# Optimization experiments

Measured on AMD Instinct MI355X. Metric: run time of the kernel, lower is better.

## Reference

```python
import jax, jax.numpy as jnp
import numpy as np

C = 768
HEADS = 12

def setup_inputs() -> dict:
    key = jax.random.key(0)
    k1, k2, k3 = jax.random.split(key, 3)
    x = jax.random.normal(k1, (8, C, 32, 32), dtype=jnp.float32)
    # 1x1 convs are channel-wise linear maps; store as [out_c, in_c]
    w_qkv = jax.random.normal(k2, (3 * C, C), dtype=jnp.float32) * (C ** -0.5)
    w_proj = jax.random.normal(k3, (C, C), dtype=jnp.float32) * (C ** -0.5)
    return {"x": x, "w_qkv": w_qkv, "w_proj": w_proj}

def reference(x, w_qkv, w_proj):
    b, c, h, w = x.shape
    heads = HEADS
    dh = c // heads
    n = h * w
    scale = dh ** -0.5
    # 1x1 conv QKV: [b, 3c, h, w] -> [b, 3, heads, dh, n]
    qkv = jnp.einsum('oc,bchw->bohw', w_qkv, x).reshape(b, 3, heads, dh, n)
    q, k, v = qkv[:, 0], qkv[:, 1], qkv[:, 2]  # each [b, heads, dh, n]
    attn = jnp.einsum('bhdn,bhdm->bhnm', q, k) * scale  # [b, heads, n, n]
    attn = jax.nn.softmax(attn, axis=-1)
    out = jnp.einsum('bhnm,bhdm->bhdn', attn, v)  # [b, heads, dh, n]
    out = out.reshape(b, c, h, w)
    return jnp.einsum('oc,bchw->bohw', w_proj, out)
```

## Files before the change

### kernel.cpp

```cpp
#include <hip/hip_runtime.h>

typedef unsigned short u16;
typedef unsigned int u32;
typedef float v4f __attribute__((ext_vector_type(4)));
typedef __bf16 bf16x8 __attribute__((ext_vector_type(8)));

#define BATCH 8
#define CDIM 768
#define NHEAD 12
#define DH 64
#define NSEQ 1024
#define SCL 0.18033688011112042f

__device__ __forceinline__ u16 f2bf(float f) {
  u32 u = __builtin_bit_cast(u32, f);
  u += 0x7fffu + ((u >> 16) & 1u);
  return (u16)(u >> 16);
}

__device__ __forceinline__ u16 b16(float f) {
  return (u16)((__builtin_bit_cast(u32, f) + 0x8000u) >> 16);
}
__device__ __forceinline__ u32 pkbf(float hi, float lo) {
  u32 a = __builtin_bit_cast(u32, hi) + 0x8000u;
  u32 b = __builtin_bit_cast(u32, lo) + 0x8000u;
  return __builtin_amdgcn_perm(a, b, 0x07060302u);
}

__device__ __forceinline__ v4f mfma16(bf16x8 a, bf16x8 b, v4f c) {
  return __builtin_amdgcn_mfma_f32_16x16x32_bf16(a, b, c, 0, 0, 0);
}

__device__ __forceinline__ void gload16(const u16* g, u16* l) {
  __builtin_amdgcn_global_load_lds(
      (const __attribute__((address_space(1))) void*)g,
      (__attribute__((address_space(3))) void*)l, 16, 0, 0);
}

__global__ __launch_bounds__(256) void k_prep(const float* __restrict__ x,
                                              const float* __restrict__ wq,
                                              const float* __restrict__ wp,
                                              u16* __restrict__ xT,
                                              u16* __restrict__ wqb,
                                              u16* __restrict__ wpb) {
  __shared__ u16 Ts[64][72];
  int bid = blockIdx.x;
  int t = threadIdx.x;
  if (bid < 2304) {
    bool isQ = bid < 1728;
    const float* s = isQ ? wq : wp;
    u16* d = isQ ? wqb : wpb;
    int i = (isQ ? bid : bid - 1728) * 256 + t;
    float4 v = ((const float4*)s)[i];
    u32 lo = (u32)f2bf(v.x) | ((u32)f2bf(v.y) << 16);
    u32 hi = (u32)f2bf(v.z) | ((u32)f2bf(v.w) << 16);
    ((uint2*)d)[i] = uint2{lo, hi};
    return;
  }
  int id = bid - 2304;
  int p0 = (id & 15) * 64; id >>= 4;
  int c0 = (id % 12) * 64; int b = id / 12;
  int cr = t >> 4;
  int p4 = (t & 15) * 4;
  const float* src = x + ((size_t)b * CDIM + c0) * NSEQ + p0;
#pragma unroll
  for (int i = 0; i < 4; ++i) {
    int c = cr + i * 16;
    float4 v = *(const float4*)&src[(size_t)c * NSEQ + p4];
    Ts[p4 + 0][c] = f2bf(v.x);
    Ts[p4 + 1][c] = f2bf(v.y);
    Ts[p4 + 2][c] = f2bf(v.z);
    Ts[p4 + 3][c] = f2bf(v.w);
  }
  __syncthreads();
  int p = t >> 2;
  int cq = t & 3;
  u16* dst = xT + ((size_t)b * NSEQ + p0 + p) * CDIM + c0;
#pragma unroll
  for (int j = 0; j < 2; ++j) {
    int ch = cq + j * 4;
    *(int4*)&dst[ch * 8] = *(const int4*)&Ts[p][ch * 8];
  }
}

__global__ __launch_bounds__(256) void k_gemm_qkv(const u16* __restrict__ Wb,
                                                  const u16* __restrict__ xT,
                                                  u16* __restrict__ qkT,
                                                  u16* __restrict__ vbuf) {
  int oT = blockIdx.x * 128, pT = blockIdx.y * 128, b = blockIdx.z;
  __shared__ u16 As[2][128 * 32];
  __shared__ u16 Bs[2][128 * 32];
  int t = threadIdx.x, lane = t & 63, wid = t >> 6;
  int ln = lane & 15, quad = lane >> 4;
  int wr = wid >> 1, wc = wid & 1;
  v4f acc[4][4] = {};

  int lr = lane >> 2, lc = (lane & 3) * 8;
  const u16* Ag = Wb + (size_t)(oT + wid * 16 + lr) * CDIM + lc;
  const u16* Bg = xT + ((size_t)b * NSEQ + pT + wid * 16 + lr) * CDIM + lc;
  int s0 = (wid * 16) * 32, s1 = (wid * 16 + 64) * 32;

  for (int kk = 0; kk < CDIM; kk += 64) {
    __syncthreads();
    gload16(Ag + kk, &As[0][s0]);
    gload16(Ag + (size_t)64 * CDIM + kk, &As[0][s1]);
    gload16(Ag + kk + 32, &As[1][s0]);
    gload16(Ag + (size_t)64 * CDIM + kk + 32, &As[1][s1]);
    gload16(Bg + kk, &Bs[0][s0]);
    gload16(Bg + (size_t)64 * CDIM + kk, &Bs[0][s1]);
    gload16(Bg + kk + 32, &Bs[1][s0]);
    gload16(Bg + (size_t)64 * CDIM + kk + 32, &Bs[1][s1]);
    __syncthreads();

    bf16x8 af0[4], af1[4], bf0[4], bf1[4];
#pragma unroll
    for (int mt = 0; mt < 4; ++mt) {
      af0[mt] = *(const bf16x8*)&As[0][(wr * 64 + mt * 16 + ln) * 32 + quad * 8];
      af1[mt] = *(const bf16x8*)&As[1][(wr * 64 + mt * 16 + ln) * 32 + quad * 8];
    }
#pragma unroll
    for (int nt = 0; nt < 4; ++nt) {
      bf0[nt] = *(const bf16x8*)&Bs[0][(wc * 64 + nt * 16 + ln) * 32 + quad * 8];
      bf1[nt] = *(const bf16x8*)&Bs[1][(wc * 64 + nt * 16 + ln) * 32 + quad * 8];
    }
#pragma unroll
    for (int mt = 0; mt < 4; ++mt)
#pragma unroll
      for (int nt = 0; nt < 4; ++nt) {
        acc[mt][nt] = mfma16(af0[mt], bf0[nt], acc[mt][nt]);
        acc[mt][nt] = mfma16(af1[mt], bf1[nt], acc[mt][nt]);
      }
  }

  bool isV = (oT >= 2 * CDIM);
#pragma unroll
  for (int mt = 0; mt < 4; ++mt) {
#pragma unroll
    for (int nt = 0; nt < 4; ++nt) {
      int ro = oT + wr * 64 + mt * 16 + quad * 4;
      int cp = pT + wc * 64 + nt * 16 + ln;
      if (!isV) {
        u32 lo = (u32)f2bf(acc[mt][nt][0]) | ((u32)f2bf(acc[mt][nt][1]) << 16);
        u32 hi = (u32)f2bf(acc[mt][nt][2]) | ((u32)f2bf(acc[mt][nt][3]) << 16);
        *(uint2*)&qkT[((size_t)b * NSEQ + cp) * 1536 + ro] = uint2{lo, hi};
      } else {
#pragma unroll
        for (int r = 0; r < 4; ++r)
          vbuf[((size_t)b * CDIM + (ro - 2 * CDIM + r)) * NSEQ + cp] =
              f2bf(acc[mt][nt][r]);
      }
    }
  }
}

__global__ __launch_bounds__(256) void k_attn(const u16* __restrict__ qkT,
                                              const u16* __restrict__ vbuf,
                                              u16* __restrict__ attnT) {
  int id = blockIdx.x;
  int b = id & 7;
  int j = id >> 3;
  int h = j % 12;
  int nt0 = (j / 12) * 128;

  int t = threadIdx.x, lane = t & 63, wid = t >> 6;
  int ln = lane & 15, quad = lane >> 4;
  int nbase = nt0 + wid * 32;

  __shared__ u16 Ks[2][2][64 * 32];
  __shared__ u16 Vs[2][2][64 * 32];
  __shared__ u16 Pa[4][32 * 72];
  u16* myP = Pa[wid];

  const u16* qbase = qkT + ((size_t)b * NSEQ + nbase) * 1536 + h * DH;
  bf16x8 aq[2][2];
#pragma unroll
  for (int mt = 0; mt < 2; ++mt)
#pragma unroll
    for (int ks = 0; ks < 2; ++ks)
      aq[mt][ks] = *(const bf16x8*)&qbase[(size_t)(mt * 16 + ln) * 1536 + ks * 32 + quad * 8];

  bf16x8 ones;
#pragma unroll
  for (int i = 0; i < 8; ++i) ones[i] = __builtin_bit_cast(__bf16, (u16)0x3F80);

  v4f oacc[2][4] = {};
  v4f lacc[2] = {};

  int lr = lane >> 2, lc = (lane & 3) * 8;
  const u16* kgw = qkT + (size_t)b * NSEQ * 1536 + CDIM + h * DH +
                   (size_t)(wid * 16 + lr) * 1536 + lc;
  const u16* vgw = vbuf + ((size_t)b * CDIM + h * DH + wid * 16 + lr) * NSEQ + lc;
  int sb = (wid * 16) * 32;

  gload16(kgw, &Ks[0][0][sb]);
  gload16(kgw + 32, &Ks[0][1][sb]);
  gload16(vgw, &Vs[0][0][sb]);
  gload16(vgw + 32, &Vs[0][1][sb]);
  __syncthreads();

  for (int s = 0; s < 16; ++s) {
    int cur = s & 1, nxt = cur ^ 1;
    if (s < 15) {
      size_t ko = (size_t)(s + 1) * 64 * 1536;
      int vo = (s + 1) * 64;
      gload16(kgw + ko, &Ks[nxt][0][sb]);
      gload16(kgw + ko + 32, &Ks[nxt][1][sb]);
      gload16(vgw + vo, &Vs[nxt][0][sb]);
      gload16(vgw + vo + 32, &Vs[nxt][1][sb]);
    }

#pragma unroll
    for (int ct = 0; ct < 4; ++ct) {
      bf16x8 kf0 = *(const bf16x8*)&Ks[cur][0][(ct * 16 + ln) * 32 + quad * 8];
      bf16x8 kf1 = *(const bf16x8*)&Ks[cur][1][(ct * 16 + ln) * 32 + quad * 8];
#pragma unroll
      for (int mt = 0; mt < 2; ++mt) {
        v4f sc = {};
        sc = mfma16(kf0, aq[mt][0], sc);
        sc = mfma16(kf1, aq[mt][1], sc);
        float p0 = __builtin_amdgcn_exp2f(sc[0] * SCL);
        float p1 = __builtin_amdgcn_exp2f(sc[1] * SCL);
        float p2 = __builtin_amdgcn_exp2f(sc[2] * SCL);
        float p3 = __builtin_amdgcn_exp2f(sc[3] * SCL);
        *(uint2*)&myP[(mt * 16 + ln) * 72 + ct * 16 + quad * 4] =
            uint2{pkbf(p1, p0), pkbf(p3, p2)};
      }
    }

    bf16x8 ap[2][2];
#pragma unroll
    for (int mt = 0; mt < 2; ++mt)
#pragma unroll
      for (int ks = 0; ks < 2; ++ks)
        ap[mt][ks] = *(const bf16x8*)&myP[(mt * 16 + ln) * 72 + ks * 32 + quad * 8];
#pragma unroll
    for (int mt = 0; mt < 2; ++mt) {
      lacc[mt] = mfma16(ap[mt][0], ones, lacc[mt]);
      lacc[mt] = mfma16(ap[mt][1], ones, lacc[mt]);
    }
#pragma unroll
    for (int nt = 0; nt < 4; ++nt) {
      bf16x8 vf0 = *(const bf16x8*)&Vs[cur][0][(nt * 16 + ln) * 32 + quad * 8];
      bf16x8 vf1 = *(const bf16x8*)&Vs[cur][1][(nt * 16 + ln) * 32 + quad * 8];
#pragma unroll
      for (int mt = 0; mt < 2; ++mt) {
        oacc[mt][nt] = mfma16(ap[mt][0], vf0, oacc[mt][nt]);
        oacc[mt][nt] = mfma16(ap[mt][1], vf1, oacc[mt][nt]);
      }
    }
    __syncthreads();
  }

#pragma unroll
  for (int mt = 0; mt < 2; ++mt) {
#pragma unroll
    for (int r = 0; r < 4; ++r) {
      float inv = 1.0f / lacc[mt][r];
      int n = nbase + mt * 16 + quad * 4 + r;
      u16* dst = attnT + ((size_t)b * NSEQ + n) * CDIM + h * DH;
#pragma unroll
      for (int nt = 0; nt < 4; ++nt)
        dst[nt * 16 + ln] = b16(oacc[mt][nt][r] * inv);
    }
  }
}

__global__ __launch_bounds__(256) void k_gemm_proj(const u16* __restrict__ Wb,
                                                   const u16* __restrict__ aT,
                                                   float* __restrict__ out) {
  int b = blockIdx.x, oT = blockIdx.y * 128, pT = blockIdx.z * 128;
  __shared__ u16 As[2][128 * 32];
  __shared__ u16 Bs[2][128 * 32];
  int t = threadIdx.x, lane = t & 63, wid = t >> 6;
  int ln = lane & 15, quad = lane >> 4;
  int wr = wid >> 1, wc = wid & 1;
  v4f acc[4][4] = {};

  int lr = lane >> 2, lc = (lane & 3) * 8;
  const u16* Ag = Wb + (size_t)(oT + wid * 16 + lr) * CDIM + lc;
  const u16* Bg = aT + ((size_t)b * NSEQ + pT + wid * 16 + lr) * CDIM + lc;
  int s0 = (wid * 16) * 32, s1 = (wid * 16 + 64) * 32;

  for (int kk = 0; kk < CDIM; kk += 64) {
    __syncthreads();
    gload16(Ag + kk, &As[0][s0]);
    gload16(Ag + (size_t)64 * CDIM + kk, &As[0][s1]);
    gload16(Ag + kk + 32, &As[1][s0]);
    gload16(Ag + (size_t)64 * CDIM + kk + 32, &As[1][s1]);
    gload16(Bg + kk, &Bs[0][s0]);
    gload16(Bg + (size_t)64 * CDIM + kk, &Bs[0][s1]);
    gload16(Bg + kk + 32, &Bs[1][s0]);
    gload16(Bg + (size_t)64 * CDIM + kk + 32, &Bs[1][s1]);
    __syncthreads();

    bf16x8 af0[4], af1[4], bf0[4], bf1[4];
#pragma unroll
    for (int mt = 0; mt < 4; ++mt) {
      af0[mt] = *(const bf16x8*)&As[0][(wr * 64 + mt * 16 + ln) * 32 + quad * 8];
      af1[mt] = *(const bf16x8*)&As[1][(wr * 64 + mt * 16 + ln) * 32 + quad * 8];
    }
#pragma unroll
    for (int nt = 0; nt < 4; ++nt) {
      bf0[nt] = *(const bf16x8*)&Bs[0][(wc * 64 + nt * 16 + ln) * 32 + quad * 8];
      bf1[nt] = *(const bf16x8*)&Bs[1][(wc * 64 + nt * 16 + ln) * 32 + quad * 8];
    }
#pragma unroll
    for (int mt = 0; mt < 4; ++mt)
#pragma unroll
      for (int nt = 0; nt < 4; ++nt) {
        acc[mt][nt] = mfma16(af0[mt], bf0[nt], acc[mt][nt]);
        acc[mt][nt] = mfma16(af1[mt], bf1[nt], acc[mt][nt]);
      }
  }

#pragma unroll
  for (int mt = 0; mt < 4; ++mt) {
#pragma unroll
    for (int nt = 0; nt < 4; ++nt) {
      int ro = oT + wr * 64 + mt * 16 + quad * 4;
      int cp = pT + wc * 64 + nt * 16 + ln;
#pragma unroll
      for (int r = 0; r < 4; ++r)
        out[((size_t)b * CDIM + ro + r) * NSEQ + cp] = acc[mt][nt][r];
    }
  }
}

extern "C" void kernel_launch(void* const* d_in, const int* in_sizes, int n_in,
                              void* d_out, int out_size, void* d_ws, size_t ws_size,
                              hipStream_t stream) {
  const float* x = (const float*)d_in[0];
  const float* w_qkv = (const float*)d_in[1];
  const float* w_proj = (const float*)d_in[2];
  float* out = (float*)d_out;

  char* ws = (char*)d_ws;
  u16* wqkv_bf = (u16*)(ws);
  u16* wproj_bf = (u16*)(ws + 3538944);
  u16* xT = (u16*)(ws + 4718592);
  u16* vbuf = (u16*)(ws + 17301504);
  u16* qkT = (u16*)d_out;
  u16* attnT = xT;

  k_prep<<<dim3(3840), dim3(256), 0, stream>>>(x, w_qkv, w_proj, xT, wqkv_bf, wproj_bf);
  k_gemm_qkv<<<dim3(18, 8, 8), dim3(256), 0, stream>>>(wqkv_bf, xT, qkT, vbuf);
  k_attn<<<dim3(768), dim3(256), 0, stream>>>(qkT, vbuf, attnT);
  k_gemm_proj<<<dim3(8, 6, 8), dim3(256), 0, stream>>>(wproj_bf, attnT, out);
}
```

Baseline: 193.0 us.

## Rewrite QKV and projection GEMMs with triple-buffered pipelined shared-memory core

Both 1x1-conv GEMMs now share one core: 512-thread blocks computing 128x256 tiles, a three-stage LDS ring filled by direct global-to-LDS loads, XOR-swizzled LDS layout against bank conflicts, split MFMA phases with raised wave priority, and explicit waitcnt/barrier scheduling. The grid is flattened with a block-index swizzle for L2 locality, and tiles may span batch boundaries. The aim is to hide global load latency behind MFMA work and raise per-block reuse. In exchange it uses about 144KB of LDS per block and relies on hand-placed waitcnt counts being correct.

Result: no change. 190.8 us (-1.2%).

```diff
diff --git a/kernel.cpp b/kernel.cpp
--- a/kernel.cpp
+++ b/kernel.cpp
@@ -21,6 +21,7 @@
 __device__ __forceinline__ u16 b16(float f) {
   return (u16)((__builtin_bit_cast(u32, f) + 0x8000u) >> 16);
 }
+
 __device__ __forceinline__ u32 pkbf(float hi, float lo) {
   u32 a = __builtin_bit_cast(u32, hi) + 0x8000u;
   u32 b = __builtin_bit_cast(u32, lo) + 0x8000u;
@@ -83,71 +84,151 @@
   }
 }
 
-__global__ __launch_bounds__(256) void k_gemm_qkv(const u16* __restrict__ Wb,
-                                                  const u16* __restrict__ xT,
-                                                  u16* __restrict__ qkT,
-                                                  u16* __restrict__ vbuf) {
-  int oT = blockIdx.x * 128, pT = blockIdx.y * 128, b = blockIdx.z;
-  __shared__ u16 As[2][128 * 32];
-  __shared__ u16 Bs[2][128 * 32];
+#define NKT 12
+
+__device__ __forceinline__ void gemm_core(const u16* __restrict__ Ag,
+                                          const u16* __restrict__ Bg,
+                                          u16* sm, v4f (&acc)[4][4]) {
   int t = threadIdx.x, lane = t & 63, wid = t >> 6;
   int ln = lane & 15, quad = lane >> 4;
-  int wr = wid >> 1, wc = wid & 1;
+  int wm = wid >> 2, wn = wid & 3;
+
+  int sr = t >> 3;
+  int sc = ((t & 7) ^ (sr & 7)) * 8;
+  const u16* As0 = Ag + (size_t)sr * CDIM + sc;
+  const u16* Bs0 = Bg + (size_t)sr * CDIM + sc;
+  int ldw = wid * 512;
+
+  int x = ln & 7;
+  int rA = (wm * 64 + ln) * 64;
+  int rB = 8192 + (wn * 64 + ln) * 64;
+  int c0 = (quad ^ x) * 8;
+  int c1 = ((4 + quad) ^ x) * 8;
+
+  {
+    u16* sb = sm;
+    gload16(As0, sb + ldw);
+    gload16(As0 + (size_t)64 * CDIM, sb + 4096 + ldw);
+    gload16(Bs0, sb + 8192 + ldw);
+    gload16(Bs0 + (size_t)64 * CDIM, sb + 12288 + ldw);
+    gload16(Bs0 + (size_t)128 * CDIM, sb + 16384 + ldw);
+    gload16(Bs0 + (size_t)192 * CDIM, sb + 20480 + ldw);
+  }
+  asm volatile("" ::: "memory");
+  {
+    u16* sb = sm + 24576;
+    const u16* Ak = As0 + 64;
+    const u16* Bk = Bs0 + 64;
+    gload16(Ak, sb + ldw);
+    gload16(Ak + (size_t)64 * CDIM, sb + 4096 + ldw);
+    gload16(Bk, sb + 8192 + ldw);
+    gload16(Bk + (size_t)64 * CDIM, sb + 12288 + ldw);
+    gload16(Bk + (size_t)128 * CDIM, sb + 16384 + ldw);
+    gload16(Bk + (size_t)192 * CDIM, sb + 20480 + ldw);
+  }
+  asm volatile("s_waitcnt vmcnt(6)" ::: "memory");
+  asm volatile("s_barrier" ::: "memory");
+
+#pragma unroll
+  for (int kt = 0; kt < NKT; ++kt) {
+    const u16* sb = sm + (kt % 3) * 24576;
+    u16* nb = sm + ((kt + 2) % 3) * 24576;
+    const u16* Ak = As0 + (kt + 2) * 64;
+    const u16* Bk = Bs0 + (kt + 2) * 64;
+
+    bf16x8 af[2][2], bfr[4][2];
+#pragma unroll
+    for (int m = 0; m < 2; ++m) {
+      af[m][0] = *(const bf16x8*)&sb[rA + m * 1024 + c0];
+      af[m][1] = *(const bf16x8*)&sb[rA + m * 1024 + c1];
+    }
+#pragma unroll
+    for (int n = 0; n < 4; ++n) {
+      bfr[n][0] = *(const bf16x8*)&sb[rB + n * 1024 + c0];
+      bfr[n][1] = *(const bf16x8*)&sb[rB + n * 1024 + c1];
+    }
+    if (kt < NKT - 2) {
+      gload16(Ak, nb + ldw);
+      gload16(Ak + (size_t)64 * CDIM, nb + 4096 + ldw);
+      gload16(Bk, nb + 8192 + ldw);
+    }
+    asm volatile("s_barrier" ::: "memory");
+    asm volatile("s_waitcnt lgkmcnt(0)" ::: "memory");
+    __builtin_amdgcn_sched_barrier(0);
+    __builtin_amdgcn_s_setprio(1);
+#pragma unroll
+    for (int m = 0; m < 2; ++m)
+#pragma unroll
+      for (int n = 0; n < 4; ++n) {
+        acc[m][n] = mfma16(af[m][0], bfr[n][0], acc[m][n]);
+        acc[m][n] = mfma16(af[m][1], bfr[n][1], acc[m][n]);
+      }
+    __builtin_amdgcn_s_setprio(0);
+    asm volatile("s_barrier" ::: "memory");
+
+#pragma unroll
+    for (int m = 0; m < 2; ++m) {
+      af[m][0] = *(const bf16x8*)&sb[rA + (m + 2) * 1024 + c0];
+      af[m][1] = *(const bf16x8*)&sb[rA + (m + 2) * 1024 + c1];
+    }
+    if (kt < NKT - 2) {
+      gload16(Bk + (size_t)64 * CDIM, nb + 12288 + ldw);
+      gload16(Bk + (size_t)128 * CDIM, nb + 16384 + ldw);
+      gload16(Bk + (size_t)192 * CDIM, nb + 20480 + ldw);
+      asm volatile("s_waitcnt vmcnt(6)" ::: "memory");
+    } else if (kt == NKT - 2) {
+      asm volatile("s_waitcnt vmcnt(0)" ::: "memory");
+    }
+    asm volatile("s_barrier" ::: "memory");
+    asm volatile("s_waitcnt lgkmcnt(0)" ::: "memory");
+    __builtin_amdgcn_sched_barrier(0);
+    __builtin_amdgcn_s_setprio(1);
+#pragma unroll
+    for (int m = 0; m < 2; ++m)
+#pragma unroll
+      for (int n = 0; n < 4; ++n) {
+        acc[m + 2][n] = mfma16(af[m][0], bfr[n][0], acc[m + 2][n]);
+        acc[m + 2][n] = mfma16(af[m][1], bfr[n][1], acc[m + 2][n]);
+      }
+    __builtin_amdgcn_s_setprio(0);
+    asm volatile("s_barrier" ::: "memory");
+  }
+}
+
+__global__ __launch_bounds__(512, 2) void k_gemm_qkv(const u16* __restrict__ Wb,
+                                                     const u16* __restrict__ xT,
+                                                     u16* __restrict__ qkT,
+                                                     u16* __restrict__ vbuf) {
+  __shared__ u16 sm[3 * 24576];
+  int bid = blockIdx.x;
+  int swz = (bid & 7) * 72 + (bid >> 3);
+  int oIdx = swz % 18, pIdx = swz / 18;
+  int oT = oIdx * 128;
+  int pG = pIdx * 256;
+
   v4f acc[4][4] = {};
-
-  int lr = lane >> 2, lc = (lane & 3) * 8;
-  const u16* Ag = Wb + (size_t)(oT + wid * 16 + lr) * CDIM + lc;
-  const u16* Bg = xT + ((size_t)b * NSEQ + pT + wid * 16 + lr) * CDIM + lc;
-  int s0 = (wid * 16) * 32, s1 = (wid * 16 + 64) * 32;
-
-  for (int kk = 0; kk < CDIM; kk += 64) {
-    __syncthreads();
-    gload16(Ag + kk, &As[0][s0]);
-    gload16(Ag + (size_t)64 * CDIM + kk, &As[0][s1]);
-    gload16(Ag + kk + 32, &As[1][s0]);
-    gload16(Ag + (size_t)64 * CDIM + kk + 32, &As[1][s1]);
-    gload16(Bg + kk, &Bs[0][s0]);
-    gload16(Bg + (size_t)64 * CDIM + kk, &Bs[0][s1]);
-    gload16(Bg + kk + 32, &Bs[1][s0]);
-    gload16(Bg + (size_t)64 * CDIM + kk + 32, &Bs[1][s1]);
-    __syncthreads();
-
-    bf16x8 af0[4], af1[4], bf0[4], bf1[4];
-#pragma unroll
-    for (int mt = 0; mt < 4; ++mt) {
-      af0[mt] = *(const bf16x8*)&As[0][(wr * 64 + mt * 16 + ln) * 32 + quad * 8];
-      af1[mt] = *(const bf16x8*)&As[1][(wr * 64 + mt * 16 + ln) * 32 + quad * 8];
-    }
-#pragma unroll
-    for (int nt = 0; nt < 4; ++nt) {
-      bf0[nt] = *(const bf16x8*)&Bs[0][(wc * 64 + nt * 16 + ln) * 32 + quad * 8];
-      bf1[nt] = *(const bf16x8*)&Bs[1][(wc * 64 + nt * 16 + ln) * 32 + quad * 8];
-    }
-#pragma unroll
-    for (int mt = 0; mt < 4; ++mt)
-#pragma unroll
-      for (int nt = 0; nt < 4; ++nt) {
-        acc[mt][nt] = mfma16(af0[mt], bf0[nt], acc[mt][nt]);
-        acc[mt][nt] = mfma16(af1[mt], bf1[nt], acc[mt][nt]);
-      }
-  }
-
-  bool isV = (oT >= 2 * CDIM);
-#pragma unroll
-  for (int mt = 0; mt < 4; ++mt) {
-#pragma unroll
-    for (int nt = 0; nt < 4; ++nt) {
-      int ro = oT + wr * 64 + mt * 16 + quad * 4;
-      int cp = pT + wc * 64 + nt * 16 + ln;
+  gemm_core(Wb + (size_t)oT * CDIM, xT + (size_t)pG * CDIM, sm, acc);
+
+  int t = threadIdx.x, lane = t & 63, wid = t >> 6;
+  int ln = lane & 15, quad = lane >> 4;
+  int wm = wid >> 2, wn = wid & 3;
+  bool isV = oT >= 2 * CDIM;
+#pragma unroll
+  for (int m = 0; m < 4; ++m) {
+#pragma unroll
+    for (int n = 0; n < 4; ++n) {
+      int ro = oT + wm * 64 + m * 16 + quad * 4;
+      int cp = pG + wn * 64 + n * 16 + ln;
+      int b = cp >> 10, p = cp & 1023;
       if (!isV) {
-        u32 lo = (u32)f2bf(acc[mt][nt][0]) | ((u32)f2bf(acc[mt][nt][1]) << 16);
-        u32 hi = (u32)f2bf(acc[mt][nt][2]) | ((u32)f2bf(acc[mt][nt][3]) << 16);
-        *(uint2*)&qkT[((size_t)b * NSEQ + cp) * 1536 + ro] = uint2{lo, hi};
+        u32 lo = (u32)f2bf(acc[m][n][0]) | ((u32)f2bf(acc[m][n][1]) << 16);
+        u32 hi = (u32)f2bf(acc[m][n][2]) | ((u32)f2bf(acc[m][n][3]) << 16);
+        *(uint2*)&qkT[((size_t)b * NSEQ + p) * 1536 + ro] = uint2{lo, hi};
       } else {
 #pragma unroll
         for (int r = 0; r < 4; ++r)
-          vbuf[((size_t)b * CDIM + (ro - 2 * CDIM + r)) * NSEQ + cp] =
-              f2bf(acc[mt][nt][r]);
+          vbuf[((size_t)b * CDIM + (ro - 2 * CDIM + r)) * NSEQ + p] =
+              f2bf(acc[m][n][r]);
       }
     }
   }
@@ -265,63 +346,32 @@
   }
 }
 
-__global__ __launch_bounds__(256) void k_gemm_proj(const u16* __restrict__ Wb,
-                                                   const u16* __restrict__ aT,
-                                                   float* __restrict__ out) {
-  int b = blockIdx.x, oT = blockIdx.y * 128, pT = blockIdx.z * 128;
-  __shared__ u16 As[2][128 * 32];
-  __shared__ u16 Bs[2][128 * 32];
+__global__ __launch_bounds__(512, 2) void k_gemm_proj(const u16* __restrict__ Wb,
+                                                      const u16* __restrict__ aT,
+                                                      float* __restrict__ out) {
+  __shared__ u16 sm[3 * 24576];
+  int bid = blockIdx.x;
+  int swz = (bid & 7) * 24 + (bid >> 3);
+  int oIdx = swz % 6, pIdx = swz / 6;
+  int oT = oIdx * 128;
+  int pG = pIdx * 256;
+
+  v4f acc[4][4] = {};
+  gemm_core(Wb + (size_t)oT * CDIM, aT + (size_t)pG * CDIM, sm, acc);
+
   int t = threadIdx.x, lane = t & 63, wid = t >> 6;
   int ln = lane & 15, quad = lane >> 4;
-  int wr = wid >> 1, wc = wid & 1;
-  v4f acc[4][4] = {};
-
-  int lr = lane >> 2, lc = (lane & 3) * 8;
-  const u16* Ag = Wb + (size_t)(oT + wid * 16 + lr) * CDIM + lc;
-  const u16* Bg = aT + ((size_t)b * NSEQ + pT + wid * 16 + lr) * CDIM + lc;
-  int s0 = (wid * 16) * 32, s1 = (wid * 16 + 64) * 32;
-
-  for (int kk = 0; kk < CDIM; kk += 64) {
-    __syncthreads();
-    gload16(Ag + kk, &As[0][s0]);
-    gload16(Ag + (size_t)64 * CDIM + kk, &As[0][s1]);
-    gload16(Ag + kk + 32, &As[1][s0]);
-    gload16(Ag + (size_t)64 * CDIM + kk + 32, &As[1][s1]);
-    gload16(Bg + kk, &Bs[0][s0]);
-    gload16(Bg + (size_t)64 * CDIM + kk, &Bs[0][s1]);
-    gload16(Bg + kk + 32, &Bs[1][s0]);
-    gload16(Bg + (size_t)64 * CDIM + kk + 32, &Bs[1][s1]);
-    __syncthreads();
-
-    bf16x8 af0[4], af1[4], bf0[4], bf1[4];
-#pragma unroll
-    for (int mt = 0; mt < 4; ++mt) {
-      af0[mt] = *(const bf16x8*)&As[0][(wr * 64 + mt * 16 + ln) * 32 + quad * 8];
-      af1[mt] = *(const bf16x8*)&As[1][(wr * 64 + mt * 16 + ln) * 32 + quad * 8];
-    }
-#pragma unroll
-    for (int nt = 0; nt < 4; ++nt) {
-      bf0[nt] = *(const bf16x8*)&Bs[0][(wc * 64 + nt * 16 + ln) * 32 + quad * 8];
-      bf1[nt] = *(const bf16x8*)&Bs[1][(wc * 64 + nt * 16 + ln) * 32 + quad * 8];
-    }
-#pragma unroll
-    for (int mt = 0; mt < 4; ++mt)
-#pragma unroll
-      for (int nt = 0; nt < 4; ++nt) {
-        acc[mt][nt] = mfma16(af0[mt], bf0[nt], acc[mt][nt]);
-        acc[mt][nt] = mfma16(af1[mt], bf1[nt], acc[mt][nt]);
-      }
-  }
-
-#pragma unroll
-  for (int mt = 0; mt < 4; ++mt) {
-#pragma unroll
-    for (int nt = 0; nt < 4; ++nt) {
-      int ro = oT + wr * 64 + mt * 16 + quad * 4;
-      int cp = pT + wc * 64 + nt * 16 + ln;
+  int wm = wid >> 2, wn = wid & 3;
+#pragma unroll
+  for (int m = 0; m < 4; ++m) {
+#pragma unroll
+    for (int n = 0; n < 4; ++n) {
+      int ro = oT + wm * 64 + m * 16 + quad * 4;
+      int cp = pG + wn * 64 + n * 16 + ln;
+      int b = cp >> 10, p = cp & 1023;
 #pragma unroll
       for (int r = 0; r < 4; ++r)
-        out[((size_t)b * CDIM + ro + r) * NSEQ + cp] = acc[mt][nt][r];
+        out[((size_t)b * CDIM + ro + r) * NSEQ + p] = acc[m][n][r];
     }
   }
 }
@@ -343,7 +393,7 @@
   u16* attnT = xT;
 
   k_prep<<<dim3(3840), dim3(256), 0, stream>>>(x, w_qkv, w_proj, xT, wqkv_bf, wproj_bf);
-  k_gemm_qkv<<<dim3(18, 8, 8), dim3(256), 0, stream>>>(wqkv_bf, xT, qkT, vbuf);
+  k_gemm_qkv<<<dim3(576), dim3(512), 0, stream>>>(wqkv_bf, xT, qkT, vbuf);
   k_attn<<<dim3(768), dim3(256), 0, stream>>>(qkT, vbuf, attnT);
-  k_gemm_proj<<<dim3(8, 6, 8), dim3(256), 0, stream>>>(wproj_bf, attnT, out);
-}
+  k_gemm_proj<<<dim3(192), dim3(512), 0, stream>>>(wproj_bf, attnT, out);
+}
```
